# Performance work log

Measured on AMD Instinct MI355X. Metric: run time of the kernel, lower is better.

The kernel has to match this reference:

```python
import jax, jax.numpy as jnp
import numpy as np

R = 4  # search_range

def setup_inputs() -> dict:
    key = jax.random.key(0)
    k1, k2 = jax.random.split(key)
    B, C, H, W = 4, 128, 96, 160
    src = jax.random.normal(k1, (B, C, H, W), dtype=jnp.float32)
    tgt = jax.random.normal(k2, (B, C, H, W), dtype=jnp.float32)
    return {"src": src, "tgt": tgt}

def _cost_volume(src, tgt):
    B, C, H, W = src.shape
    # zero-pad tgt by R on each spatial side (as in F.pad(tgt, [R]*4))
    tp = jnp.pad(tgt, ((0, 0), (0, 0), (R, R), (R, R)))
    # shifted map cropped to the central HxW window; shift (dh, dw) means
    # the neighbor at offset (dh, dw) relative to each src pixel.
    def crop(dh, dw):
        return tp[:, :, R + dh:R + dh + H, R + dw:R + dw + W]
    # order matches torch: [identity, left, right, up, down] for i=1..R
    maps = [crop(0, 0)]
    for i in range(1, R + 1):
        maps.extend([crop(-i, 0), crop(i, 0), crop(0, -i), crop(0, i)])
    neigh = jnp.stack(maps, axis=2)  # [B, C, 1+4R, H, W]
    # correlation: sum over channels -> [B, 1+4R, H, W]
    return jnp.einsum('bchw,bcshw->bshw', src, neigh)

def reference(src, tgt):
    return _cost_volume(src, tgt)
```

## Files before the change

kernel.cpp:

```cpp
#include <hip/hip_runtime.h>

#define RR 4
#define NS 17
#define BB 4
#define CC 128
#define HH 96
#define WW 160
#define HWSZ (HH * WW)

#define TW 32
#define HTILE 16
#define TH 2
#define TROWS (HTILE + 2 * RR)
#define TCOLS (TW + 2 * RR)
#define TILE_N (TROWS * TCOLS)
#define CCHUNK 32
#define NCHUNK (CC / CCHUNK)

__global__ __launch_bounds__(256, 4)
void cost_volume_kernel(const float* __restrict__ src,
                        const float* __restrict__ tgt,
                        float* __restrict__ out) {
    __shared__ float tile[TROWS][TCOLS];

    const int x   = threadIdx.x;
    const int hg  = threadIdx.y;
    const int tid = hg * TW + x;

    const int w0 = blockIdx.x * TW;
    const int h0 = blockIdx.y * HTILE;
    const int b  = blockIdx.z & 3;
    const int c0 = (blockIdx.z >> 2) * CCHUNK;

    const int w  = w0 + x;
    const int hb = h0 + hg * TH;

    float acc[TH][NS];
#pragma unroll
    for (int i = 0; i < TH; ++i)
#pragma unroll
        for (int s = 0; s < NS; ++s) acc[i][s] = 0.f;

    const float* tgt_b = tgt + (size_t)(b * CC) * HWSZ;
    const float* src_b = src + (size_t)(b * CC) * HWSZ;

    float pre[4];
    float spre[TH];

    auto fetch_tile = [&](int c, float vals[4]) {
        const float* t = tgt_b + (size_t)c * HWSZ;
#pragma unroll
        for (int k = 0; k < 4; ++k) {
            int idx = tid + k * 256;
            float v = 0.f;
            if (idx < TILE_N) {
                int r   = idx / TCOLS;
                int col = idx - r * TCOLS;
                int gr  = h0 - RR + r;
                int gc  = w0 - RR + col;
                if (gr >= 0 && gr < HH && gc >= 0 && gc < WW)
                    v = t[gr * WW + gc];
            }
            vals[k] = v;
        }
    };
    auto fetch_src = [&](int c, float vals[TH]) {
        const float* sp = src_b + (size_t)c * HWSZ + hb * WW + w;
#pragma unroll
        for (int i = 0; i < TH; ++i) vals[i] = sp[i * WW];
    };

    fetch_tile(c0, pre);
    fetch_src(c0, spre);

    for (int cc = 0; cc < CCHUNK; ++cc) {
#pragma unroll
        for (int k = 0; k < 4; ++k) {
            int idx = tid + k * 256;
            if (idx < TILE_N) ((float*)tile)[idx] = pre[k];
        }
        float sv[TH];
#pragma unroll
        for (int i = 0; i < TH; ++i) sv[i] = spre[i];
        __syncthreads();

        if (cc + 1 < CCHUNK) {
            fetch_tile(c0 + cc + 1, pre);
            fetch_src(c0 + cc + 1, spre);
        }

#pragma unroll
        for (int i = 0; i < TH; ++i) {
            const int r   = RR + hg * TH + i;
            const int col = RR + x;
            acc[i][0] = fmaf(sv[i], tile[r][col], acc[i][0]);
#pragma unroll
            for (int off = 1; off <= RR; ++off) {
                float up    = tile[r - off][col];
                float down  = tile[r + off][col];
                float left  = tile[r][col - off];
                float right = tile[r][col + off];
                acc[i][4 * off - 3] = fmaf(sv[i], up,    acc[i][4 * off - 3]);
                acc[i][4 * off - 2] = fmaf(sv[i], down,  acc[i][4 * off - 2]);
                acc[i][4 * off - 1] = fmaf(sv[i], left,  acc[i][4 * off - 1]);
                acc[i][4 * off    ] = fmaf(sv[i], right, acc[i][4 * off    ]);
            }
        }
        __syncthreads();
    }

#pragma unroll
    for (int i = 0; i < TH; ++i) {
        const int h = hb + i;
#pragma unroll
        for (int s = 0; s < NS; ++s) {
            atomicAdd(out + (((size_t)b * NS + s) * HH + h) * WW + w, acc[i][s]);
        }
    }
}

extern "C" void kernel_launch(void* const* d_in, const int* in_sizes, int n_in,
                              void* d_out, int out_size, void* d_ws, size_t ws_size,
                              hipStream_t stream) {
    const float* src = (const float*)d_in[0];
    const float* tgt = (const float*)d_in[1];
    float* out = (float*)d_out;

    hipMemsetAsync(out, 0, (size_t)out_size * sizeof(float), stream);

    dim3 block(TW, 8, 1);
    dim3 grid(WW / TW, HH / HTILE, BB * NCHUNK);
    cost_volume_kernel<<<grid, block, 0, stream>>>(src, tgt, out);
}
```

Baseline: 126.6 us.

## Compute four horizontal pixels per thread with float4 loads and register reuse

Each thread now handles four adjacent output columns of one row. It loads source and target with float4 global loads and reads a 12-wide row strip from shared memory once, then reuses it for the left and right shifts. The tile grows to 32x32 and the channel chunk shrinks from 32 to 8, which doubles the block count. The aim is to cut shared-memory reads and global load instructions per output. The cost is four times as many atomic adds into the output, because there are now more channel chunks.

```diff
diff --git a/kernel.cpp b/kernel.cpp
--- a/kernel.cpp
+++ b/kernel.cpp
@@ -9,113 +9,114 @@
 #define HWSZ (HH * WW)
 
 #define TW 32
-#define HTILE 16
-#define TH 2
-#define TROWS (HTILE + 2 * RR)
+#define THT 32
 #define TCOLS (TW + 2 * RR)
-#define TILE_N (TROWS * TCOLS)
-#define CCHUNK 32
+#define TROWS (THT + 2 * RR)
+#define NF4 (TROWS * TCOLS / 4)
+#define CCHUNK 8
 #define NCHUNK (CC / CCHUNK)
+#define F4STRIDE (HWSZ / 4)
 
-__global__ __launch_bounds__(256, 4)
+typedef float4 f4;
+
+__global__ __launch_bounds__(256, 3)
 void cost_volume_kernel(const float* __restrict__ src,
                         const float* __restrict__ tgt,
                         float* __restrict__ out) {
-    __shared__ float tile[TROWS][TCOLS];
+    __shared__ __align__(16) float tile[TROWS][TCOLS];
 
     const int x   = threadIdx.x;
-    const int hg  = threadIdx.y;
-    const int tid = hg * TW + x;
+    const int ty  = threadIdx.y;
+    const int tid = ty * 8 + x;
 
     const int w0 = blockIdx.x * TW;
-    const int h0 = blockIdx.y * HTILE;
+    const int h0 = blockIdx.y * THT;
     const int b  = blockIdx.z & 3;
     const int c0 = (blockIdx.z >> 2) * CCHUNK;
-
-    const int w  = w0 + x;
-    const int hb = h0 + hg * TH;
-
-    float acc[TH][NS];
-#pragma unroll
-    for (int i = 0; i < TH; ++i)
-#pragma unroll
-        for (int s = 0; s < NS; ++s) acc[i][s] = 0.f;
 
     const float* tgt_b = tgt + (size_t)(b * CC) * HWSZ;
     const float* src_b = src + (size_t)(b * CC) * HWSZ;
 
-    float pre[4];
-    float spre[TH];
+    const int idxA = tid, idxB = tid + 256;
+    const int rA = idxA / 10, sA = idxA - 10 * rA;
+    const int rB = idxB / 10, sB = idxB - 10 * rB;
+    const int grA = h0 - RR + rA, gcA = w0 - RR + 4 * sA;
+    const int grB = h0 - RR + rB, gcB = w0 - RR + 4 * sB;
+    const bool vA = (grA >= 0) && (grA < HH) && (gcA >= 0) && (gcA <= WW - 4);
+    const bool vB = (idxB < NF4) && (grB >= 0) && (grB < HH) && (gcB >= 0) && (gcB <= WW - 4);
+    const f4* gA = (const f4*)(tgt_b + ((size_t)c0 * HWSZ + grA * WW + gcA));
+    const f4* gB = (const f4*)(tgt_b + ((size_t)c0 * HWSZ + grB * WW + gcB));
+    const f4* gS = (const f4*)(src_b + ((size_t)c0 * HWSZ + (h0 + ty) * WW + w0 + 4 * x));
 
-    auto fetch_tile = [&](int c, float vals[4]) {
-        const float* t = tgt_b + (size_t)c * HWSZ;
+    const f4 zero4 = make_float4(0.f, 0.f, 0.f, 0.f);
+
+    float acc[NS][4];
 #pragma unroll
-        for (int k = 0; k < 4; ++k) {
-            int idx = tid + k * 256;
-            float v = 0.f;
-            if (idx < TILE_N) {
-                int r   = idx / TCOLS;
-                int col = idx - r * TCOLS;
-                int gr  = h0 - RR + r;
-                int gc  = w0 - RR + col;
-                if (gr >= 0 && gr < HH && gc >= 0 && gc < WW)
-                    v = t[gr * WW + gc];
-            }
-            vals[k] = v;
-        }
-    };
-    auto fetch_src = [&](int c, float vals[TH]) {
-        const float* sp = src_b + (size_t)c * HWSZ + hb * WW + w;
+    for (int s = 0; s < NS; ++s)
 #pragma unroll
-        for (int i = 0; i < TH; ++i) vals[i] = sp[i * WW];
-    };
+        for (int j = 0; j < 4; ++j) acc[s][j] = 0.f;
 
-    fetch_tile(c0, pre);
-    fetch_src(c0, spre);
+    f4 pA = vA ? gA[0] : zero4;
+    f4 pB = vB ? gB[0] : zero4;
+    f4 pS = gS[0];
 
     for (int cc = 0; cc < CCHUNK; ++cc) {
-#pragma unroll
-        for (int k = 0; k < 4; ++k) {
-            int idx = tid + k * 256;
-            if (idx < TILE_N) ((float*)tile)[idx] = pre[k];
-        }
-        float sv[TH];
-#pragma unroll
-        for (int i = 0; i < TH; ++i) sv[i] = spre[i];
+        ((f4*)tile)[idxA] = pA;
+        if (idxB < NF4) ((f4*)tile)[idxB] = pB;
+        float sv[4] = {pS.x, pS.y, pS.z, pS.w};
         __syncthreads();
 
         if (cc + 1 < CCHUNK) {
-            fetch_tile(c0 + cc + 1, pre);
-            fetch_src(c0 + cc + 1, spre);
+            const size_t o = (size_t)(cc + 1) * F4STRIDE;
+            pA = vA ? gA[o] : zero4;
+            pB = vB ? gB[o] : zero4;
+            pS = gS[o];
+        }
+
+        const int rr = RR + ty;
+        const int cb = 4 * x;
+
+        f4 R0 = *(const f4*)&tile[rr][cb];
+        f4 R1 = *(const f4*)&tile[rr][cb + 4];
+        f4 R2 = *(const f4*)&tile[rr][cb + 8];
+        float row[12] = {R0.x, R0.y, R0.z, R0.w,
+                         R1.x, R1.y, R1.z, R1.w,
+                         R2.x, R2.y, R2.z, R2.w};
+
+#pragma unroll
+        for (int j = 0; j < 4; ++j) acc[0][j] = fmaf(sv[j], row[4 + j], acc[0][j]);
+
+#pragma unroll
+        for (int i = 1; i <= RR; ++i) {
+            f4 up = *(const f4*)&tile[rr - i][cb + 4];
+            f4 dn = *(const f4*)&tile[rr + i][cb + 4];
+            float u[4] = {up.x, up.y, up.z, up.w};
+            float d[4] = {dn.x, dn.y, dn.z, dn.w};
+#pragma unroll
+            for (int j = 0; j < 4; ++j) {
+                acc[4 * i - 3][j] = fmaf(sv[j], u[j], acc[4 * i - 3][j]);
+                acc[4 * i - 2][j] = fmaf(sv[j], d[j], acc[4 * i - 2][j]);
+            }
         }
 
 #pragma unroll
-        for (int i = 0; i < TH; ++i) {
-            const int r   = RR + hg * TH + i;
-            const int col = RR + x;
-            acc[i][0] = fmaf(sv[i], tile[r][col], acc[i][0]);
+        for (int i = 1; i <= RR; ++i) {
 #pragma unroll
-            for (int off = 1; off <= RR; ++off) {
-                float up    = tile[r - off][col];
-                float down  = tile[r + off][col];
-                float left  = tile[r][col - off];
-                float right = tile[r][col + off];
-                acc[i][4 * off - 3] = fmaf(sv[i], up,    acc[i][4 * off - 3]);
-                acc[i][4 * off - 2] = fmaf(sv[i], down,  acc[i][4 * off - 2]);
-                acc[i][4 * off - 1] = fmaf(sv[i], left,  acc[i][4 * off - 1]);
-                acc[i][4 * off    ] = fmaf(sv[i], right, acc[i][4 * off    ]);
+            for (int j = 0; j < 4; ++j) {
+                acc[4 * i - 1][j] = fmaf(sv[j], row[4 + j - i], acc[4 * i - 1][j]);
+                acc[4 * i    ][j] = fmaf(sv[j], row[4 + j + i], acc[4 * i    ][j]);
             }
         }
         __syncthreads();
     }
 
+    const int h = h0 + ty;
+    const int wb = w0 + 4 * x;
 #pragma unroll
-    for (int i = 0; i < TH; ++i) {
-        const int h = hb + i;
+    for (int s = 0; s < NS; ++s) {
+        float* op = out + (((size_t)(b * NS + s)) * HH + h) * WW + wb;
 #pragma unroll
-        for (int s = 0; s < NS; ++s) {
-            atomicAdd(out + (((size_t)b * NS + s) * HH + h) * WW + w, acc[i][s]);
-        }
+        for (int j = 0; j < 4; ++j) atomicAdd(op + j, acc[s][j]);
     }
 }
 
@@ -128,7 +129,7 @@
 
     hipMemsetAsync(out, 0, (size_t)out_size * sizeof(float), stream);
 
-    dim3 block(TW, 8, 1);
-    dim3 grid(WW / TW, HH / HTILE, BB * NCHUNK);
+    dim3 block(8, 32, 1);
+    dim3 grid(WW / TW, HH / THT, BB * NCHUNK);
     cost_volume_kernel<<<grid, block, 0, stream>>>(src, tgt, out);
 }
```

Result: slower. 347.7 us (+174.7%).

## Stage four channels per barrier with float4 tile loads and shared vertical reuse

Applied to the files above, without the earlier changes.

The kernel now loads a group of four target channels into shared memory per sync, using float4 global loads for the haloed tile. The number of __syncthreads drops fourfold, and more loads are in flight per prefetch. In the compute loop, the ten vertical neighbours for a thread's two rows are read once into registers and shared across both rows, which cuts LDS reads. The cost is a larger shared tile (about 15 KB) and more registers for the prefetched data. Edge tiles rely on the halo columns falling on 4-aligned boundaries, where a float4 is either fully in bounds or fully out.

```diff
diff --git a/kernel.cpp b/kernel.cpp
--- a/kernel.cpp
+++ b/kernel.cpp
@@ -9,112 +9,125 @@
 #define HWSZ (HH * WW)
 
 #define TW 32
-#define HTILE 16
-#define TH 2
-#define TROWS (HTILE + 2 * RR)
-#define TCOLS (TW + 2 * RR)
-#define TILE_N (TROWS * TCOLS)
+#define THT 16
+#define TROWS 24
+#define TCOLS 40
+#define CH_F4 (TROWS * TCOLS / 4)
+#define G 4
 #define CCHUNK 32
 #define NCHUNK (CC / CCHUNK)
+#define NGROUP (CCHUNK / G)
+#define NSLOT (G * CH_F4)
+
+typedef float4 f4;
 
 __global__ __launch_bounds__(256, 4)
 void cost_volume_kernel(const float* __restrict__ src,
                         const float* __restrict__ tgt,
                         float* __restrict__ out) {
-    __shared__ float tile[TROWS][TCOLS];
+    __shared__ __align__(16) float tile[G][TROWS][TCOLS];
 
     const int x   = threadIdx.x;
-    const int hg  = threadIdx.y;
-    const int tid = hg * TW + x;
+    const int ty  = threadIdx.y;
+    const int tid = ty * TW + x;
 
     const int w0 = blockIdx.x * TW;
-    const int h0 = blockIdx.y * HTILE;
+    const int h0 = blockIdx.y * THT;
     const int b  = blockIdx.z & 3;
     const int c0 = (blockIdx.z >> 2) * CCHUNK;
-
-    const int w  = w0 + x;
-    const int hb = h0 + hg * TH;
-
-    float acc[TH][NS];
-#pragma unroll
-    for (int i = 0; i < TH; ++i)
-#pragma unroll
-        for (int s = 0; s < NS; ++s) acc[i][s] = 0.f;
 
     const float* tgt_b = tgt + (size_t)(b * CC) * HWSZ;
     const float* src_b = src + (size_t)(b * CC) * HWSZ;
 
-    float pre[4];
-    float spre[TH];
+    int  soff[4];
+    bool sval[4];
+#pragma unroll
+    for (int k = 0; k < 4; ++k) {
+        int s   = tid + k * 256;
+        int ch  = s / CH_F4;
+        int idx = s - ch * CH_F4;
+        int r   = idx / 10;
+        int c   = idx - 10 * r;
+        int gr  = h0 - RR + r;
+        int gc  = w0 - RR + 4 * c;
+        sval[k] = (s < NSLOT) && (gr >= 0) && (gr < HH) && (gc >= 0) && (gc <= WW - 4);
+        soff[k] = ch * HWSZ + gr * WW + gc;
+    }
+    const float* srow = src_b + (h0 + 2 * ty) * WW + (w0 + x);
+    const f4 zero4 = make_float4(0.f, 0.f, 0.f, 0.f);
 
-    auto fetch_tile = [&](int c, float vals[4]) {
-        const float* t = tgt_b + (size_t)c * HWSZ;
+    float acc[2][NS];
+#pragma unroll
+    for (int i = 0; i < 2; ++i)
+#pragma unroll
+        for (int s = 0; s < NS; ++s) acc[i][s] = 0.f;
+
+    f4 P[4];
+    float S[G][2];
+
+    auto load_group = [&](int g) {
+        const float* tg = tgt_b + (size_t)(c0 + g * G) * HWSZ;
+#pragma unroll
+        for (int k = 0; k < 4; ++k)
+            P[k] = sval[k] ? *(const f4*)(tg + soff[k]) : zero4;
+        const float* sg = srow + (size_t)(c0 + g * G) * HWSZ;
+#pragma unroll
+        for (int ch = 0; ch < G; ++ch) {
+            S[ch][0] = sg[(size_t)ch * HWSZ];
+            S[ch][1] = sg[(size_t)ch * HWSZ + WW];
+        }
+    };
+
+    load_group(0);
+
+    for (int g = 0; g < NGROUP; ++g) {
 #pragma unroll
         for (int k = 0; k < 4; ++k) {
-            int idx = tid + k * 256;
-            float v = 0.f;
-            if (idx < TILE_N) {
-                int r   = idx / TCOLS;
-                int col = idx - r * TCOLS;
-                int gr  = h0 - RR + r;
-                int gc  = w0 - RR + col;
-                if (gr >= 0 && gr < HH && gc >= 0 && gc < WW)
-                    v = t[gr * WW + gc];
-            }
-            vals[k] = v;
+            int s = tid + k * 256;
+            if (s < NSLOT) ((f4*)tile)[s] = P[k];
         }
-    };
-    auto fetch_src = [&](int c, float vals[TH]) {
-        const float* sp = src_b + (size_t)c * HWSZ + hb * WW + w;
+        float sc[G][2];
 #pragma unroll
-        for (int i = 0; i < TH; ++i) vals[i] = sp[i * WW];
-    };
-
-    fetch_tile(c0, pre);
-    fetch_src(c0, spre);
-
-    for (int cc = 0; cc < CCHUNK; ++cc) {
-#pragma unroll
-        for (int k = 0; k < 4; ++k) {
-            int idx = tid + k * 256;
-            if (idx < TILE_N) ((float*)tile)[idx] = pre[k];
-        }
-        float sv[TH];
-#pragma unroll
-        for (int i = 0; i < TH; ++i) sv[i] = spre[i];
+        for (int ch = 0; ch < G; ++ch) { sc[ch][0] = S[ch][0]; sc[ch][1] = S[ch][1]; }
         __syncthreads();
 
-        if (cc + 1 < CCHUNK) {
-            fetch_tile(c0 + cc + 1, pre);
-            fetch_src(c0 + cc + 1, spre);
-        }
+        if (g + 1 < NGROUP) load_group(g + 1);
 
 #pragma unroll
-        for (int i = 0; i < TH; ++i) {
-            const int r   = RR + hg * TH + i;
-            const int col = RR + x;
-            acc[i][0] = fmaf(sv[i], tile[r][col], acc[i][0]);
+        for (int ch = 0; ch < G; ++ch) {
+            float v[10];
 #pragma unroll
-            for (int off = 1; off <= RR; ++off) {
-                float up    = tile[r - off][col];
-                float down  = tile[r + off][col];
-                float left  = tile[r][col - off];
-                float right = tile[r][col + off];
-                acc[i][4 * off - 3] = fmaf(sv[i], up,    acc[i][4 * off - 3]);
-                acc[i][4 * off - 2] = fmaf(sv[i], down,  acc[i][4 * off - 2]);
-                acc[i][4 * off - 1] = fmaf(sv[i], left,  acc[i][4 * off - 1]);
-                acc[i][4 * off    ] = fmaf(sv[i], right, acc[i][4 * off    ]);
+            for (int k = 0; k < 10; ++k) v[k] = tile[ch][2 * ty + k][RR + x];
+#pragma unroll
+            for (int i = 0; i < 2; ++i) {
+                const float sv = sc[ch][i];
+                acc[i][0] = fmaf(sv, v[4 + i], acc[i][0]);
+#pragma unroll
+                for (int off = 1; off <= RR; ++off) {
+                    acc[i][4 * off - 3] = fmaf(sv, v[4 + i - off], acc[i][4 * off - 3]);
+                    acc[i][4 * off - 2] = fmaf(sv, v[4 + i + off], acc[i][4 * off - 2]);
+                }
+            }
+#pragma unroll
+            for (int i = 0; i < 2; ++i) {
+                const float sv = sc[ch][i];
+                const float* row = &tile[ch][RR + 2 * ty + i][RR + x];
+#pragma unroll
+                for (int off = 1; off <= RR; ++off) {
+                    acc[i][4 * off - 1] = fmaf(sv, row[-off], acc[i][4 * off - 1]);
+                    acc[i][4 * off    ] = fmaf(sv, row[ off], acc[i][4 * off    ]);
+                }
             }
         }
         __syncthreads();
     }
 
 #pragma unroll
-    for (int i = 0; i < TH; ++i) {
-        const int h = hb + i;
+    for (int i = 0; i < 2; ++i) {
+        const int h = h0 + 2 * ty + i;
 #pragma unroll
         for (int s = 0; s < NS; ++s) {
-            atomicAdd(out + (((size_t)b * NS + s) * HH + h) * WW + w, acc[i][s]);
+            atomicAdd(out + (((size_t)(b * NS + s)) * HH + h) * WW + w0 + x, acc[i][s]);
         }
     }
 }
@@ -129,6 +142,6 @@
     hipMemsetAsync(out, 0, (size_t)out_size * sizeof(float), stream);
 
     dim3 block(TW, 8, 1);
-    dim3 grid(WW / TW, HH / HTILE, BB * NCHUNK);
+    dim3 grid(WW / TW, HH / THT, BB * NCHUNK);
     cost_volume_kernel<<<grid, block, 0, stream>>>(src, tgt, out);
 }
```

Result: slower. 132.2 us (+4.4%).
